# Optimization experiments

Measured on AMD Instinct MI355X. Metric: run time of the kernel, lower is better.

## Reference

```python
import jax, jax.numpy as jnp
import numpy as np

B, S, V, E, H = 256, 64, 30000, 300, 512
D_A, R, C, P = 350, 8, 150, 16
NUM_ITERS = 3
EPS = 1e-9


def _xavier(k, shape, fi, fo):
    lim = (6.0 / (fi + fo)) ** 0.5
    return jax.random.uniform(k, shape, minval=-lim, maxval=lim, dtype=jnp.float32)


def setup_inputs() -> dict:
    key = jax.random.key(0)
    ks = jax.random.split(key, 14)
    u = 1.0 / (H ** 0.5)
    uni = lambda k, shp: jax.random.uniform(k, shp, minval=-u, maxval=u, dtype=jnp.float32)
    return {
        'input_x': jax.random.randint(ks[0], (B, S), 0, V, dtype=jnp.int32),
        'lens': jnp.full((B,), S, dtype=jnp.int32),
        'embedding': jax.random.normal(ks[1], (V, E), dtype=jnp.float32) * 0.1,
        'w_ih_f': uni(ks[2], (4 * H, E)), 'w_hh_f': uni(ks[3], (4 * H, H)),
        'b_ih_f': uni(ks[4], (4 * H,)), 'b_hh_f': uni(ks[5], (4 * H,)),
        'w_ih_b': uni(ks[6], (4 * H, E)), 'w_hh_b': uni(ks[7], (4 * H, H)),
        'b_ih_b': uni(ks[8], (4 * H,)), 'b_hh_b': uni(ks[9], (4 * H,)),
        'ws1': _xavier(ks[10], (D_A, 2 * H), 2 * H, D_A),
        'ws2': _xavier(ks[11], (R, D_A), D_A, R),
        'capsule_weights': _xavier(ks[12], (R, 2 * H, C * P), 2 * H, C * P),
    }


def _lstm_dir(x, w_ih, w_hh, b_ih, b_hh, reverse):
    # x: [S, B, E] -> hidden states [S, B, H] (torch gate order i, f, g, o)
    b = x.shape[1]
    def step(carry, xt):
        h, c = carry
        z = xt @ w_ih.T + h @ w_hh.T + (b_ih + b_hh)
        i, f, g, o = jnp.split(z, 4, axis=-1)
        c = jax.nn.sigmoid(f) * c + jax.nn.sigmoid(i) * jnp.tanh(g)
        h = jax.nn.sigmoid(o) * jnp.tanh(c)
        return (h, c), h
    init = (jnp.zeros((b, H), x.dtype), jnp.zeros((b, H), x.dtype))
    _, hs = jax.lax.scan(step, init, x, reverse=reverse)
    return hs


def _squash(s):
    # tool.squash: (|s|^2 / (1+|s|^2)) * s / |s|
    n2 = jnp.sum(s * s, axis=-1, keepdims=True)
    return (n2 / (1.0 + n2)) * s / jnp.sqrt(n2 + EPS)


def _forward(input_x, embedding, w_ih_f, w_hh_f, b_ih_f, b_hh_f,
             w_ih_b, w_hh_b, b_ih_b, b_hh_b, ws1, ws2, capsule_weights):
    # embed; torch transposes [B,S] -> [S,B] then embeds -> [S,B,E]
    emb = embedding[input_x.T]
    # bidirectional LSTM (lens == S, so pack/pad is identity)
    h_fwd = _lstm_dir(emb, w_ih_f, w_hh_f, b_ih_f, b_hh_f, reverse=False)
    h_bwd = _lstm_dir(emb, w_ih_b, w_hh_b, b_ih_b, b_hh_b, reverse=True)
    output = jnp.transpose(jnp.concatenate([h_fwd, h_bwd], axis=-1), (1, 0, 2))  # [B,S,2H]
    # structured self-attention (dropout is identity at p=0 / eval)
    pre = jnp.tanh(jnp.einsum('bsd,ad->bsa', output, ws1))          # [B,S,d_a]
    att = jnp.einsum('bsa,ra->brs', pre, ws2)                        # [B,r,S]
    attention = jax.nn.softmax(att, axis=-1)
    semantic = jnp.einsum('brs,bsd->brd', attention, output)         # [B,r,2H]
    # prediction vectors: sum_d semantic[b,r,d] * W[r,d,k]
    pred = jnp.einsum('brd,rdk->brk', semantic, capsule_weights)
    pred = pred.reshape(-1, R, C, P)                                 # [B,r,C,P]
    # dynamic routing
    logits = jnp.zeros((pred.shape[0], R, C), pred.dtype)
    routes = None
    v = None
    for _ in range(NUM_ITERS):
        routes = jax.nn.softmax(logits, axis=2)                      # [B,r,C]
        preact = jnp.einsum('brc,brcp->bcp', routes, pred)           # [B,C,P]
        v = _squash(preact)
        logits = logits + jnp.einsum('brcp,bcp->brc', pred, v)
    class_logits = jnp.linalg.norm(v, axis=-1)                       # [B,C]
    return attention, class_logits, pred, routes


def reference(input_x, lens, embedding, w_ih_f, w_hh_f, b_ih_f, b_hh_f,
              w_ih_b, w_hh_b, b_ih_b, b_hh_b, ws1, ws2, capsule_weights):
    del lens  # all lengths == S: pack/pad identity
    return _forward(input_x, embedding, w_ih_f, w_hh_f, b_ih_f, b_hh_f,
                    w_ih_b, w_hh_b, b_ih_b, b_hh_b, ws1, ws2, capsule_weights)
```

## Files before the change

### kernel.cpp

```cpp
#include <hip/hip_runtime.h>
#include <hip/hip_bf16.h>
#include <hip/hip_cooperative_groups.h>
#include <math.h>

#define BB 256
#define SS 64
#define EE 300
#define EPX 320
#define KP 832
#define VV 30000
#define HH 512
#define H2 1024
#define DA 350
#define RR 8
#define CC 150
#define PP 16
#define CP 2400
#define NFLAG (SS * 2 * 4)

#define ATT_OFF    0L
#define CL_OFF     131072L
#define PRED_OFF   169472L
#define ROUTES_OFF 5084672L

typedef _Float16 f16;
typedef f16  f16x8 __attribute__((ext_vector_type(8)));
typedef f16  f16x4 __attribute__((ext_vector_type(4)));
typedef float f32x4 __attribute__((ext_vector_type(4)));

static __device__ __forceinline__ float sigmM(float x) { return 1.0f / (1.0f + expf(-x)); }

#define NG_ ((long)SS * BB * EPX)
#define NW_ ((long)2 * 2048 * KP)
#define NS_ ((long)384 * 1024)
__global__ __launch_bounds__(256) void m_stage(
    const int* __restrict__ ids, const float* __restrict__ emb,
    const float* __restrict__ wihF, const float* __restrict__ whhF,
    const float* __restrict__ wihB, const float* __restrict__ whhB,
    const float* __restrict__ ws1,
    f16* __restrict__ X16, f16* __restrict__ W16, f16* __restrict__ ws1_16,
    unsigned* __restrict__ flags)
{
    const long idx = (long)blockIdx.x * 256 + threadIdx.x;
    if (idx < NG_) {
        const int e = (int)(idx % EPX);
        const int row = (int)(idx / EPX);
        const int s = row >> 8, b = row & 255;
        int tok = ids[(long)b * SS + s];
        if ((unsigned)tok >= (unsigned)VV) tok = 0;
        X16[idx] = (e < EE) ? (f16)emb[(long)tok * EE + e] : (f16)0.0f;
    } else if (idx < NG_ + NW_) {
        const long i2 = idx - NG_;
        const int dir = (int)(i2 / (2048 * KP));
        const int rem = (int)(i2 % (2048 * KP));
        const int j = rem / KP, k = rem % KP;
        const float* wih = dir ? wihB : wihF;
        const float* whh = dir ? whhB : whhF;
        float v;
        if (k < EE)        v = wih[(long)j * EE + k];
        else if (k < EPX)  v = 0.0f;
        else               v = whh[(long)j * HH + (k - EPX)];
        W16[i2] = (f16)v;
    } else if (idx < NG_ + NW_ + NS_) {
        const long i3 = idx - NG_ - NW_;
        const int j = (int)(i3 >> 10);
        ws1_16[i3] = (j < DA) ? (f16)ws1[i3] : (f16)0.0f;
    } else if (idx < NG_ + NW_ + NS_ + NFLAG) {
        flags[idx - NG_ - NW_ - NS_] = 0u;
    }
}

__global__ __launch_bounds__(256) void m_packcapsT(
    const float* __restrict__ caps, f16* __restrict__ capsT)
{
    __shared__ float t[32][33];
    const int r = blockIdx.z, k0 = blockIdx.x * 32, n0 = blockIdx.y * 32;
    const int tx = threadIdx.x & 31, ty = threadIdx.x >> 5;
    #pragma unroll
    for (int p = 0; p < 4; ++p) {
        const int k = k0 + ty + p * 8;
        const int n = n0 + tx;
        t[ty + p * 8][tx] = (n < CP) ? caps[((long)r * H2 + k) * CP + n] : 0.0f;
    }
    __syncthreads();
    #pragma unroll
    for (int p = 0; p < 4; ++p) {
        const int n = n0 + ty + p * 8;
        if (n < 2432)
            capsT[((long)r * 2432 + n) * H2 + k0 + tx] = (f16)t[tx][ty + p * 8];
    }
}

__global__ __launch_bounds__(512, 1) void p_lstm7(
    const f16* __restrict__ X16, f16* __restrict__ hs16,
    f16* __restrict__ hx, unsigned* __restrict__ flags,
    const f16* __restrict__ W16,
    const float* __restrict__ bihF, const float* __restrict__ bhhF,
    const float* __restrict__ bihB, const float* __restrict__ bhhB)
{
    __shared__ f16 Wl[4 * 26 * 64 * 8];
    __shared__ f32x4 part[4][64][4];
    __shared__ f16 hstage[64][16];

    const int bid = blockIdx.x;
    const int dir = bid & 1;
    const int bq  = (bid >> 1) & 3;
    const int ut  = bid >> 3;
    const int u0  = ut * 16;
    const int b0  = bq * 64;
    const int tid = threadIdx.x;
    const int wave = tid >> 6, lane = tid & 63;
    const int bt = wave & 3, kh = wave >> 2;
    const int l15 = lane & 15;
    const int kgrp = (lane >> 4) * 8;

    {
        const f16* Wsrc = W16 + (long)dir * 2048 * KP;
        for (int f = tid; f < 4 * 26 * 64; f += 512) {
            const int g  = f / (26 * 64);
            const int rm = f % (26 * 64);
            const int kt = rm >> 6, ln = rm & 63;
            const long src = ((long)g * HH + u0 + (ln & 15)) * KP + kt * 32 + ((ln >> 4) * 8);
            *(f16x8*)(Wl + (long)f * 8) = *(const f16x8*)(Wsrc + src);
        }
    }
    __syncthreads();

    const int arow = b0 + bt * 16 + l15;
    const int u = u0 + l15;
    const float* bi = dir ? bihB : bihF;
    const float* bh = dir ? bhhB : bhhF;
    const float bias0 = bi[u]          + bh[u];
    const float bias1 = bi[HH + u]     + bh[HH + u];
    const float bias2 = bi[2 * HH + u] + bh[2 * HH + u];
    const float bias3 = bi[3 * HH + u] + bh[3 * HH + u];
    const int rbase = (lane >> 4) * 4;
    float cc[4] = {0.f, 0.f, 0.f, 0.f};

    f32x4 xacc[4];
    const int xb = kh ? 5 : 0;
    auto computeX = [&](int se) {
        #pragma unroll
        for (int g = 0; g < 4; ++g) xacc[g] = (f32x4){0.f, 0.f, 0.f, 0.f};
        const f16* Xrow = X16 + ((long)se * BB + arow) * EPX;
        #pragma unroll
        for (int j = 0; j < 5; ++j) {
            const int kt = xb + j;
            const int k0 = kt * 32 + kgrp;
            const f16x8 afr = *(const f16x8*)(Xrow + k0);
            #pragma unroll
            for (int g = 0; g < 4; ++g) {
                const f16x8 bfr = *(const f16x8*)(Wl + (((g * 26 + kt) << 6) + lane) * 8);
                xacc[g] = __builtin_amdgcn_mfma_f32_16x16x32_f16(afr, bfr, xacc[g], 0, 0, 0);
            }
        }
    };
    computeX(dir ? (SS - 1) : 0);

    const int hb = kh ? 8 : 0;
    for (int s = 0; s < SS; ++s) {
        const int s_eff = dir ? (SS - 1 - s) : s;

        if (s > 0) {
            if (tid == 0) {
                const int fi = ((s - 1) * 2 + dir) * 4 + bq;
                int guard = 0;
                while (__hip_atomic_load(&flags[fi], __ATOMIC_RELAXED,
                                         __HIP_MEMORY_SCOPE_AGENT) < 32u) {
                    __builtin_amdgcn_s_sleep(1);
                    if (++guard > (1 << 22)) break;
                }
            }
            __syncthreads();
        }

        f32x4 acc[4];
        #pragma unroll
        for (int g = 0; g < 4; ++g) acc[g] = xacc[g];

        if (s > 0) {
            const f16* hrow = hx + ((((long)((s - 1) & 1) * 2 + dir) * BB) + arow) * HH;
            unsigned long long q0[8], q1[8];
            #pragma unroll
            for (int j = 0; j < 8; ++j) {
                const unsigned long long* hp =
                    (const unsigned long long*)(hrow + (hb + j) * 32 + kgrp);
                q0[j] = __hip_atomic_load(hp,     __ATOMIC_RELAXED, __HIP_MEMORY_SCOPE_AGENT);
                q1[j] = __hip_atomic_load(hp + 1, __ATOMIC_RELAXED, __HIP_MEMORY_SCOPE_AGENT);
            }
            #pragma unroll
            for (int j = 0; j < 8; ++j) {
                const int kt = 10 + hb + j;
                union { unsigned long long q[2]; f16x8 v; } uu;
                uu.q[0] = q0[j]; uu.q[1] = q1[j];
                #pragma unroll
                for (int g = 0; g < 4; ++g) {
                    const f16x8 bfr = *(const f16x8*)(Wl + (((g * 26 + kt) << 6) + lane) * 8);
                    acc[g] = __builtin_amdgcn_mfma_f32_16x16x32_f16(uu.v, bfr, acc[g], 0, 0, 0);
                }
            }
        }

        if (kh == 1) {
            #pragma unroll
            for (int g = 0; g < 4; ++g) part[bt][lane][g] = acc[g];
        }
        __syncthreads();
        if (kh == 0) {
            #pragma unroll
            for (int g = 0; g < 4; ++g) acc[g] += part[bt][lane][g];
            #pragma unroll
            for (int i = 0; i < 4; ++i) {
                const float zi = acc[0][i] + bias0;
                const float zf = acc[1][i] + bias1;
                const float zg = acc[2][i] + bias2;
                const float zo = acc[3][i] + bias3;
                cc[i] = sigmM(zf) * cc[i] + sigmM(zi) * tanhf(zg);
                hstage[bt * 16 + rbase + i][l15] = (f16)(sigmM(zo) * tanhf(cc[i]));
            }
        }
        __syncthreads();

        {
            f16* hxw = hx + (((long)(s & 1) * 2 + dir) * BB) * HH;
            if (tid < 256) {
                const int row = tid >> 2, ch = tid & 3;
                union { unsigned long long q; f16 h4[4]; } pk;
                pk.h4[0] = hstage[row][ch * 4 + 0];
                pk.h4[1] = hstage[row][ch * 4 + 1];
                pk.h4[2] = hstage[row][ch * 4 + 2];
                pk.h4[3] = hstage[row][ch * 4 + 3];
                __hip_atomic_store(
                    (unsigned long long*)(hxw + (long)(b0 + row) * HH + u0 + ch * 4),
                    pk.q, __ATOMIC_RELAXED, __HIP_MEMORY_SCOPE_AGENT);
            }
            asm volatile("s_waitcnt vmcnt(0)" ::: "memory");
        }
        __syncthreads();
        if (tid == 0)
            __hip_atomic_fetch_add(&flags[(s * 2 + dir) * 4 + bq], 1u,
                                   __ATOMIC_RELAXED, __HIP_MEMORY_SCOPE_AGENT);

        if (tid < 256) {
            const int row = tid >> 2, ch = tid & 3;
            union { unsigned long long q; f16 h4[4]; } pk;
            pk.h4[0] = hstage[row][ch * 4 + 0];
            pk.h4[1] = hstage[row][ch * 4 + 1];
            pk.h4[2] = hstage[row][ch * 4 + 2];
            pk.h4[3] = hstage[row][ch * 4 + 3];
            *(unsigned long long*)(hs16 + ((long)(b0 + row) * SS + s_eff) * H2
                                   + dir * HH + u0 + ch * 4) = pk.q;
        }

        if (s + 1 < SS) computeX(dir ? (SS - 2 - s) : (s + 1));
    }
}

__global__ __launch_bounds__(256) void m_preG(
    const f16* __restrict__ hs16, const f16* __restrict__ ws1_16,
    f16* __restrict__ pre16)
{
    const int n0 = blockIdx.x * 192;
    const int m0 = blockIdx.y * 64;
    const int tid = threadIdx.x;
    const int wave = tid >> 6, lane = tid & 63;
    const int l15 = lane & 15;
    const int kgrp = (lane >> 4) * 8;
    const f16* Arow = hs16 + (long)(m0 + wave * 16 + l15) * H2;

    f32x4 acc[12];
    #pragma unroll
    for (int nt = 0; nt < 12; ++nt) acc[nt] = (f32x4){0.f, 0.f, 0.f, 0.f};

    for (int kt = 0; kt < 32; ++kt) {
        const int k0 = kt * 32 + kgrp;
        const f16x8 afr = *(const f16x8*)(Arow + k0);
        #pragma unroll
        for (int nt = 0; nt < 12; ++nt) {
            const f16x8 bfr = *(const f16x8*)(ws1_16 + (long)(n0 + nt * 16 + l15) * H2 + k0);
            acc[nt] = __builtin_amdgcn_mfma_f32_16x16x32_f16(afr, bfr, acc[nt], 0, 0, 0);
        }
    }

    const int rbase = (lane >> 4) * 4;
    #pragma unroll
    for (int nt = 0; nt < 12; ++nt) {
        const int n = n0 + nt * 16 + l15;
        if (n < DA) {
            #pragma unroll
            for (int i = 0; i < 4; ++i) {
                const int m = m0 + wave * 16 + rbase + i;
                pre16[(long)m * DA + n] = (f16)tanhf(acc[nt][i]);
            }
        }
    }
}

__global__ __launch_bounds__(256) void m_attsem(
    const f16* __restrict__ pre16, const float* __restrict__ ws2,
    const f16* __restrict__ hs16,
    float* __restrict__ att_out, f16* __restrict__ sem16)
{
    __shared__ f16 preS[SS * DA];
    __shared__ float w2S[RR * DA];
    __shared__ float logS[RR * SS];
    __shared__ float aS[RR * SS];
    __shared__ float rmax[RR], rsum[RR];
    const int b = blockIdx.x, tid = threadIdx.x;
    {
        const unsigned long long* src =
            (const unsigned long long*)(pre16 + (long)b * SS * DA);
        unsigned long long* dst = (unsigned long long*)preS;
        for (int i = tid; i < SS * DA / 4; i += 256) dst[i] = src[i];
    }
    for (int i = tid; i < RR * DA; i += 256) w2S[i] = ws2[i];
    __syncthreads();
    for (int pp = tid; pp < RR * SS; pp += 256) {
        const int r = pp >> 6, s = pp & 63;
        const f16* prow = &preS[s * DA];
        const float* wrow = &w2S[r * DA];
        float a = 0.0f;
        for (int k = 0; k < DA; ++k) a = fmaf((float)prow[k], wrow[k], a);
        logS[r * SS + s] = a;
    }
    __syncthreads();
    if (tid < RR) {
        float mx = -1e30f;
        for (int s = 0; s < SS; ++s) mx = fmaxf(mx, logS[tid * SS + s]);
        float sm = 0.0f;
        for (int s = 0; s < SS; ++s) sm += expf(logS[tid * SS + s] - mx);
        rmax[tid] = mx; rsum[tid] = sm;
    }
    __syncthreads();
    for (int pp = tid; pp < RR * SS; pp += 256) {
        const int r = pp >> 6;
        const float v = expf(logS[pp] - rmax[r]) / rsum[r];
        att_out[(long)b * RR * SS + pp] = v;
        aS[pp] = v;
    }
    __syncthreads();

    const int d0 = tid * 4;
    float acc[RR][4] = {};
    const f16* hb = hs16 + (long)b * SS * H2;
    for (int s = 0; s < SS; ++s) {
        const f16x4 hv = *(const f16x4*)(hb + s * H2 + d0);
        const float h0 = hv[0], h1 = hv[1], h2 = hv[2], h3 = hv[3];
        #pragma unroll
        for (int r = 0; r < RR; ++r) {
            const float a = aS[r * SS + s];
            acc[r][0] = fmaf(a, h0, acc[r][0]);
            acc[r][1] = fmaf(a, h1, acc[r][1]);
            acc[r][2] = fmaf(a, h2, acc[r][2]);
            acc[r][3] = fmaf(a, h3, acc[r][3]);
        }
    }
    #pragma unroll
    for (int r = 0; r < RR; ++r) {
        f16x4 o; o[0] = (f16)acc[r][0]; o[1] = (f16)acc[r][1];
        o[2] = (f16)acc[r][2]; o[3] = (f16)acc[r][3];
        *(f16x4*)(sem16 + ((long)b * RR + r) * H2 + d0) = o;
    }
}

__global__ __launch_bounds__(512) void m_predG(
    const f16* __restrict__ sem16, const f16* __restrict__ capsT16,
    float* __restrict__ pred_out)
{
    const int n0 = blockIdx.x * 64;
    const int r  = blockIdx.y;
    const int tid = threadIdx.x;
    const int wave = tid >> 6, lane = tid & 63;
    const int l15 = lane & 15;
    const int kgrp = (lane >> 4) * 8;
    const f16* Bp = capsT16 + (long)r * 2432 * H2;
    const f16* A0 = sem16 + ((long)(wave * 32 + l15) * RR + r) * H2;

    f32x4 acc[2][4];
    #pragma unroll
    for (int mt = 0; mt < 2; ++mt)
        #pragma unroll
        for (int nt = 0; nt < 4; ++nt) acc[mt][nt] = (f32x4){0.f, 0.f, 0.f, 0.f};

    for (int kt = 0; kt < 32; ++kt) {
        const int k0 = kt * 32 + kgrp;
        const f16x8 a0 = *(const f16x8*)(A0 + k0);
        const f16x8 a1 = *(const f16x8*)(A0 + (long)16 * RR * H2 + k0);
        #pragma unroll
        for (int nt = 0; nt < 4; ++nt) {
            const f16x8 bfr = *(const f16x8*)(Bp + (long)(n0 + nt * 16 + l15) * H2 + k0);
            acc[0][nt] = __builtin_amdgcn_mfma_f32_16x16x32_f16(a0, bfr, acc[0][nt], 0, 0, 0);
            acc[1][nt] = __builtin_amdgcn_mfma_f32_16x16x32_f16(a1, bfr, acc[1][nt], 0, 0, 0);
        }
    }

    const int rbase = (lane >> 4) * 4;
    #pragma unroll
    for (int mt = 0; mt < 2; ++mt) {
        #pragma unroll
        for (int nt = 0; nt < 4; ++nt) {
            const int n = n0 + nt * 16 + l15;
            if (n < CP) {
                #pragma unroll
                for (int i = 0; i < 4; ++i) {
                    const int m = wave * 32 + mt * 16 + rbase + i;
                    pred_out[((long)m * RR + r) * CP + n] = acc[mt][nt][i];
                }
            }
        }
    }
}

__global__ __launch_bounds__(512) void m_route(
    const float* __restrict__ pred,
    float* __restrict__ cls_out, float* __restrict__ routes_out)
{
    __shared__ float predS[RR * CP];
    __shared__ float logitS[RR * CC];
    __shared__ float routeS[RR * CC];
    __shared__ float preactS[CP];
    __shared__ float vS[CP];
    __shared__ float scaleS[CC];
    __shared__ float rmax[RR], rsum[RR];
    const int b = blockIdx.x, tid = threadIdx.x;
    const float* ps = pred + (long)b * RR * CP;
    for (int i = tid; i < RR * CP; i += 512) predS[i] = ps[i];
    for (int i = tid; i < RR * CC; i += 512) logitS[i] = 0.0f;
    __syncthreads();

    for (int it = 0; it < 3; ++it) {
        if (tid < RR) {
            float mx = -1e30f;
            for (int c = 0; c < CC; ++c) mx = fmaxf(mx, logitS[tid * CC + c]);
            float sm = 0.0f;
            for (int c = 0; c < CC; ++c) sm += expf(logitS[tid * CC + c] - mx);
            rmax[tid] = mx; rsum[tid] = sm;
        }
        __syncthreads();
        for (int i = tid; i < RR * CC; i += 512) {
            const int r = i / CC;
            routeS[i] = expf(logitS[i] - rmax[r]) / rsum[r];
        }
        __syncthreads();
        for (int cp = tid; cp < CP; cp += 512) {
            const int c = cp >> 4;
            float a = 0.0f;
            #pragma unroll
            for (int r = 0; r < RR; ++r)
                a = fmaf(routeS[r * CC + c], predS[r * CP + cp], a);
            preactS[cp] = a;
        }
        __syncthreads();
        for (int c = tid; c < CC; c += 512) {
            float n2 = 0.0f;
            #pragma unroll
            for (int p = 0; p < PP; ++p) { const float x = preactS[c * PP + p]; n2 = fmaf(x, x, n2); }
            scaleS[c] = (n2 / (1.0f + n2)) / sqrtf(n2 + 1e-9f);
        }
        __syncthreads();
        for (int cp = tid; cp < CP; cp += 512) vS[cp] = preactS[cp] * scaleS[cp >> 4];
        __syncthreads();
        for (int i = tid; i < RR * CC; i += 512) {
            const int r = i / CC, c = i % CC;
            float a = 0.0f;
            #pragma unroll
            for (int p = 0; p < PP; ++p)
                a = fmaf(predS[r * CP + c * PP + p], vS[c * PP + p], a);
            logitS[i] += a;
        }
        __syncthreads();
    }

    for (int i = tid; i < RR * CC; i += 512)
        routes_out[(long)b * RR * CC + i] = routeS[i];
    for (int c = tid; c < CC; c += 512) {
        float n2 = 0.0f;
        #pragma unroll
        for (int p = 0; p < PP; ++p) { const float x = vS[c * PP + p]; n2 = fmaf(x, x, n2); }
        cls_out[(long)b * CC + c] = sqrtf(n2);
    }
}

extern "C" void kernel_launch(void* const* d_in, const int* in_sizes, int n_in,
                              void* d_out, int out_size, void* d_ws, size_t ws_size,
                              hipStream_t stream)
{
    (void)in_sizes; (void)n_in; (void)out_size;
    const int*   ids   = (const int*)d_in[0];
    const float* emb   = (const float*)d_in[2];
    const float* wih_f = (const float*)d_in[3];
    const float* whh_f = (const float*)d_in[4];
    const float* bih_f = (const float*)d_in[5];
    const float* bhh_f = (const float*)d_in[6];
    const float* wih_b = (const float*)d_in[7];
    const float* whh_b = (const float*)d_in[8];
    const float* bih_b = (const float*)d_in[9];
    const float* bhh_b = (const float*)d_in[10];
    const float* ws1   = (const float*)d_in[11];
    const float* ws2   = (const float*)d_in[12];
    const float* caps  = (const float*)d_in[13];
    float* out = (float*)d_out;

    float* ws = (float*)d_ws;
    f16*  hs16   = (f16*)ws;
    f16*  hx     = (f16*)(ws + 8388608);
    f16*  X16    = (f16*)(ws + 8650752);
    f16*  W16    = (f16*)(ws + 11272192);
    f16*  ws1_16 = (f16*)(ws + 12976128);
    f16*  sem16  = (f16*)(ws + 13172736);
    unsigned* flags = (unsigned*)(ws + 14221312);
    f16*  pre16  = X16;
    f16*  capsT16 = (f16*)ws;
    const size_t need = (size_t)(14221312 + 512) * 4;
    if (ws_size < need) return;

    {
        const long total = NG_ + NW_ + NS_ + NFLAG;
        m_stage<<<(int)((total + 255) / 256), 256, 0, stream>>>(
            ids, emb, wih_f, whh_f, wih_b, whh_b, ws1, X16, W16, ws1_16, flags);
    }

    {
        const f16* a0 = X16; f16* a1 = hs16; f16* a2 = hx; unsigned* a3 = flags;
        const f16* a4 = W16;
        const float* a5 = bih_f; const float* a6 = bhh_f;
        const float* a7 = bih_b; const float* a8 = bhh_b;
        void* kargs[] = {(void*)&a0, (void*)&a1, (void*)&a2, (void*)&a3, (void*)&a4,
                         (void*)&a5, (void*)&a6, (void*)&a7, (void*)&a8};
        hipLaunchCooperativeKernel((void*)p_lstm7, dim3(256), dim3(512),
                                   kargs, 0, stream);
    }

    m_preG<<<dim3(2, 256), 256, 0, stream>>>(hs16, ws1_16, pre16);

    m_attsem<<<BB, 256, 0, stream>>>(pre16, ws2, hs16, out + ATT_OFF, sem16);

    m_packcapsT<<<dim3(32, 76, 8), 256, 0, stream>>>(caps, capsT16);

    m_predG<<<dim3(38, 8), 512, 0, stream>>>(sem16, capsT16, out + PRED_OFF);

    m_route<<<BB, 512, 0, stream>>>(out + PRED_OFF, out + CL_OFF, out + ROUTES_OFF);
}
```

Before: 853.6 us.

## Replace shared atomic counter with per-block padded step flags in LSTM barrier

The cross-block step barrier in the persistent LSTM kernel previously used one atomic counter per (step, direction, batch quarter), which 32 blocks incremented and a single thread polled. Now each block stores its completed step number into its own cache-line-padded flag, and a whole wave polls the 32 peer flags in parallel and waits until all of them reach the current step. This is meant to remove contention on a single atomic address and shorten barrier latency on the serial recurrence. The change also transposes the shared partial-sum buffer layout to avoid bank conflicts and interleaves the h loads with the MFMAs instead of batching them first, which may reduce latency hiding.

```diff
diff --git a/kernel.cpp b/kernel.cpp
--- a/kernel.cpp
+++ b/kernel.cpp
@@ -16,7 +16,7 @@
 #define CC 150
 #define PP 16
 #define CP 2400
-#define NFLAG (SS * 2 * 4)
+#define NPF 4096
 
 #define ATT_OFF    0L
 #define CL_OFF     131072L
@@ -28,18 +28,18 @@
 typedef f16  f16x4 __attribute__((ext_vector_type(4)));
 typedef float f32x4 __attribute__((ext_vector_type(4)));
 
-static __device__ __forceinline__ float sigmM(float x) { return 1.0f / (1.0f + expf(-x)); }
+static __device__ __forceinline__ float sigmN(float x) { return 1.0f / (1.0f + expf(-x)); }
 
 #define NG_ ((long)SS * BB * EPX)
 #define NW_ ((long)2 * 2048 * KP)
 #define NS_ ((long)384 * 1024)
-__global__ __launch_bounds__(256) void m_stage(
+__global__ __launch_bounds__(256) void n_stage(
     const int* __restrict__ ids, const float* __restrict__ emb,
     const float* __restrict__ wihF, const float* __restrict__ whhF,
     const float* __restrict__ wihB, const float* __restrict__ whhB,
     const float* __restrict__ ws1,
     f16* __restrict__ X16, f16* __restrict__ W16, f16* __restrict__ ws1_16,
-    unsigned* __restrict__ flags)
+    unsigned* __restrict__ pflag)
 {
     const long idx = (long)blockIdx.x * 256 + threadIdx.x;
     if (idx < NG_) {
@@ -65,12 +65,12 @@
         const long i3 = idx - NG_ - NW_;
         const int j = (int)(i3 >> 10);
         ws1_16[i3] = (j < DA) ? (f16)ws1[i3] : (f16)0.0f;
-    } else if (idx < NG_ + NW_ + NS_ + NFLAG) {
-        flags[idx - NG_ - NW_ - NS_] = 0u;
-    }
-}
-
-__global__ __launch_bounds__(256) void m_packcapsT(
+    } else if (idx < NG_ + NW_ + NS_ + NPF) {
+        pflag[idx - NG_ - NW_ - NS_] = 0u;
+    }
+}
+
+__global__ __launch_bounds__(256) void n_packcapsT(
     const float* __restrict__ caps, f16* __restrict__ capsT)
 {
     __shared__ float t[32][33];
@@ -91,15 +91,15 @@
     }
 }
 
-__global__ __launch_bounds__(512, 1) void p_lstm7(
+__global__ __launch_bounds__(512, 1) void p_lstm8(
     const f16* __restrict__ X16, f16* __restrict__ hs16,
-    f16* __restrict__ hx, unsigned* __restrict__ flags,
+    f16* __restrict__ hx, unsigned* __restrict__ pflag,
     const f16* __restrict__ W16,
     const float* __restrict__ bihF, const float* __restrict__ bhhF,
     const float* __restrict__ bihB, const float* __restrict__ bhhB)
 {
     __shared__ f16 Wl[4 * 26 * 64 * 8];
-    __shared__ f32x4 part[4][64][4];
+    __shared__ f32x4 part[4][4][64];
     __shared__ f16 hstage[64][16];
 
     const int bid = blockIdx.x;
@@ -113,6 +113,8 @@
     const int bt = wave & 3, kh = wave >> 2;
     const int l15 = lane & 15;
     const int kgrp = (lane >> 4) * 8;
+    const int grp32 = (dir * 4 + bq) * 32;
+    unsigned* myflag = pflag + (grp32 + ut) * 16;
 
     {
         const f16* Wsrc = W16 + (long)dir * 2048 * KP;
@@ -162,12 +164,15 @@
         const int s_eff = dir ? (SS - 1 - s) : s;
 
         if (s > 0) {
-            if (tid == 0) {
-                const int fi = ((s - 1) * 2 + dir) * 4 + bq;
+            if (wave == 0) {
+                const unsigned* fp = pflag + (grp32 + (lane & 31)) * 16;
                 int guard = 0;
-                while (__hip_atomic_load(&flags[fi], __ATOMIC_RELAXED,
-                                         __HIP_MEMORY_SCOPE_AGENT) < 32u) {
+                unsigned v = __hip_atomic_load(fp, __ATOMIC_RELAXED,
+                                               __HIP_MEMORY_SCOPE_AGENT);
+                while (!__all((int)(v >= (unsigned)s))) {
                     __builtin_amdgcn_s_sleep(1);
+                    v = __hip_atomic_load(fp, __ATOMIC_RELAXED,
+                                          __HIP_MEMORY_SCOPE_AGENT);
                     if (++guard > (1 << 22)) break;
                 }
             }
@@ -180,19 +185,14 @@
 
         if (s > 0) {
             const f16* hrow = hx + ((((long)((s - 1) & 1) * 2 + dir) * BB) + arow) * HH;
-            unsigned long long q0[8], q1[8];
-            #pragma unroll
-            for (int j = 0; j < 8; ++j) {
-                const unsigned long long* hp =
-                    (const unsigned long long*)(hrow + (hb + j) * 32 + kgrp);
-                q0[j] = __hip_atomic_load(hp,     __ATOMIC_RELAXED, __HIP_MEMORY_SCOPE_AGENT);
-                q1[j] = __hip_atomic_load(hp + 1, __ATOMIC_RELAXED, __HIP_MEMORY_SCOPE_AGENT);
-            }
             #pragma unroll
             for (int j = 0; j < 8; ++j) {
                 const int kt = 10 + hb + j;
+                const int hk = (hb + j) * 32 + kgrp;
                 union { unsigned long long q[2]; f16x8 v; } uu;
-                uu.q[0] = q0[j]; uu.q[1] = q1[j];
+                const unsigned long long* hp = (const unsigned long long*)(hrow + hk);
+                uu.q[0] = __hip_atomic_load(hp,     __ATOMIC_RELAXED, __HIP_MEMORY_SCOPE_AGENT);
+                uu.q[1] = __hip_atomic_load(hp + 1, __ATOMIC_RELAXED, __HIP_MEMORY_SCOPE_AGENT);
                 #pragma unroll
                 for (int g = 0; g < 4; ++g) {
                     const f16x8 bfr = *(const f16x8*)(Wl + (((g * 26 + kt) << 6) + lane) * 8);
@@ -203,20 +203,20 @@
 
         if (kh == 1) {
             #pragma unroll
-            for (int g = 0; g < 4; ++g) part[bt][lane][g] = acc[g];
+            for (int g = 0; g < 4; ++g) part[bt][g][lane] = acc[g];
         }
         __syncthreads();
         if (kh == 0) {
             #pragma unroll
-            for (int g = 0; g < 4; ++g) acc[g] += part[bt][lane][g];
+            for (int g = 0; g < 4; ++g) acc[g] += part[bt][g][lane];
             #pragma unroll
             for (int i = 0; i < 4; ++i) {
                 const float zi = acc[0][i] + bias0;
                 const float zf = acc[1][i] + bias1;
                 const float zg = acc[2][i] + bias2;
                 const float zo = acc[3][i] + bias3;
-                cc[i] = sigmM(zf) * cc[i] + sigmM(zi) * tanhf(zg);
-                hstage[bt * 16 + rbase + i][l15] = (f16)(sigmM(zo) * tanhf(cc[i]));
+                cc[i] = sigmN(zf) * cc[i] + sigmN(zi) * tanhf(zg);
+                hstage[bt * 16 + rbase + i][l15] = (f16)(sigmN(zo) * tanhf(cc[i]));
             }
         }
         __syncthreads();
@@ -238,8 +238,8 @@
         }
         __syncthreads();
         if (tid == 0)
-            __hip_atomic_fetch_add(&flags[(s * 2 + dir) * 4 + bq], 1u,
-                                   __ATOMIC_RELAXED, __HIP_MEMORY_SCOPE_AGENT);
+            __hip_atomic_store(myflag, (unsigned)(s + 1),
+                               __ATOMIC_RELAXED, __HIP_MEMORY_SCOPE_AGENT);
 
         if (tid < 256) {
             const int row = tid >> 2, ch = tid & 3;
@@ -256,7 +256,7 @@
     }
 }
 
-__global__ __launch_bounds__(256) void m_preG(
+__global__ __launch_bounds__(256) void n_preG(
     const f16* __restrict__ hs16, const f16* __restrict__ ws1_16,
     f16* __restrict__ pre16)
 {
@@ -296,7 +296,7 @@
     }
 }
 
-__global__ __launch_bounds__(256) void m_attsem(
+__global__ __launch_bounds__(256) void n_attsem(
     const f16* __restrict__ pre16, const float* __restrict__ ws2,
     const f16* __restrict__ hs16,
     float* __restrict__ att_out, f16* __restrict__ sem16)
@@ -363,7 +363,7 @@
     }
 }
 
-__global__ __launch_bounds__(512) void m_predG(
+__global__ __launch_bounds__(512) void n_predG(
     const f16* __restrict__ sem16, const f16* __restrict__ capsT16,
     float* __restrict__ pred_out)
 {
@@ -411,7 +411,7 @@
     }
 }
 
-__global__ __launch_bounds__(512) void m_route(
+__global__ __launch_bounds__(512) void n_route(
     const float* __restrict__ pred,
     float* __restrict__ cls_out, float* __restrict__ routes_out)
 {
@@ -508,36 +508,36 @@
     f16*  W16    = (f16*)(ws + 11272192);
     f16*  ws1_16 = (f16*)(ws + 12976128);
     f16*  sem16  = (f16*)(ws + 13172736);
-    unsigned* flags = (unsigned*)(ws + 14221312);
+    unsigned* pflag = (unsigned*)(ws + 14221312);
     f16*  pre16  = X16;
     f16*  capsT16 = (f16*)ws;
-    const size_t need = (size_t)(14221312 + 512) * 4;
+    const size_t need = (size_t)(14221312 + NPF) * 4;
     if (ws_size < need) return;
 
     {
-        const long total = NG_ + NW_ + NS_ + NFLAG;
-        m_stage<<<(int)((total + 255) / 256), 256, 0, stream>>>(
-            ids, emb, wih_f, whh_f, wih_b, whh_b, ws1, X16, W16, ws1_16, flags);
+        const long total = NG_ + NW_ + NS_ + NPF;
+        n_stage<<<(int)((total + 255) / 256), 256, 0, stream>>>(
+            ids, emb, wih_f, whh_f, wih_b, whh_b, ws1, X16, W16, ws1_16, pflag);
     }
 
     {
-        const f16* a0 = X16; f16* a1 = hs16; f16* a2 = hx; unsigned* a3 = flags;
+        const f16* a0 = X16; f16* a1 = hs16; f16* a2 = hx; unsigned* a3 = pflag;
         const f16* a4 = W16;
         const float* a5 = bih_f; const float* a6 = bhh_f;
         const float* a7 = bih_b; const float* a8 = bhh_b;
         void* kargs[] = {(void*)&a0, (void*)&a1, (void*)&a2, (void*)&a3, (void*)&a4,
                          (void*)&a5, (void*)&a6, (void*)&a7, (void*)&a8};
-        hipLaunchCooperativeKernel((void*)p_lstm7, dim3(256), dim3(512),
+        hipLaunchCooperativeKernel((void*)p_lstm8, dim3(256), dim3(512),
                                    kargs, 0, stream);
     }
 
-    m_preG<<<dim3(2, 256), 256, 0, stream>>>(hs16, ws1_16, pre16);
-
-    m_attsem<<<BB, 256, 0, stream>>>(pre16, ws2, hs16, out + ATT_OFF, sem16);
-
-    m_packcapsT<<<dim3(32, 76, 8), 256, 0, stream>>>(caps, capsT16);
-
-    m_predG<<<dim3(38, 8), 512, 0, stream>>>(sem16, capsT16, out + PRED_OFF);
-
-    m_route<<<BB, 512, 0, stream>>>(out + PRED_OFF, out + CL_OFF, out + ROUTES_OFF);
-}
+    n_preG<<<dim3(2, 256), 256, 0, stream>>>(hs16, ws1_16, pre16);
+
+    n_attsem<<<BB, 256, 0, stream>>>(pre16, ws2, hs16, out + ATT_OFF, sem16);
+
+    n_packcapsT<<<dim3(32, 76, 8), 256, 0, stream>>>(caps, capsT16);
+
+    n_predG<<<dim3(38, 8), 512, 0, stream>>>(sem16, capsT16, out + PRED_OFF);
+
+    n_route<<<BB, 512, 0, stream>>>(out + PRED_OFF, out + CL_OFF, out + ROUTES_OFF);
+}
```

After: 782.4 us. 1.09x faster.
